# Optimization experiments

Measured on AMD Instinct MI355X. Metric: run time of the kernel, lower is better.

## Reference

```python
import jax, jax.numpy as jnp
import numpy as np

NUM_HEADS = 8

def setup_inputs() -> dict:
    key = jax.random.key(0)
    k1, k2, k3 = jax.random.split(key, 3)
    B, N, C = 4, 4096, 512
    x = jax.random.normal(k1, (B, N, C), dtype=jnp.float32)
    w_qkv = jax.random.normal(k2, (C, 3 * C), dtype=jnp.float32) * (1.0 / np.sqrt(C))
    w_proj = jax.random.normal(k3, (C, C), dtype=jnp.float32) * (1.0 / np.sqrt(C))
    b_proj = jnp.zeros((C,), dtype=jnp.float32)
    return {"x": x, "w_qkv": w_qkv, "w_proj": w_proj, "b_proj": b_proj}

def reference(x, w_qkv, w_proj, b_proj):
    B, N, C = x.shape
    H = NUM_HEADS
    D = C // H
    # qkv projection (no bias), split into q, k, v of shape [B, H, N, D]
    qkv = (x @ w_qkv).reshape(B, N, 3, H, D)
    qkv = jnp.transpose(qkv, (2, 0, 3, 1, 4))
    q, k, v = qkv[0], qkv[1], qkv[2]
    # q: softmax over head_dim; k: elu(k)+1 then softmax over sequence dim
    q = jax.nn.softmax(q, axis=-1)
    k = jax.nn.softmax(jax.nn.elu(k) + 1.0, axis=-2)
    # linear attention: context = k^T @ v  -> [B, H, D, D]
    context = jnp.einsum('bhnd,bhne->bhde', k, v)
    # out = q @ context -> [B, H, N, D]
    out = jnp.einsum('bhnd,bhde->bhne', q, context)
    out = jnp.transpose(out, (0, 2, 1, 3)).reshape(B, N, C)
    # output projection (dropout with p=0.0 is identity)
    return out @ w_proj + b_proj
```

## Files before the change

kernel.cpp:

```cpp
#include <hip/hip_runtime.h>
#include <hip/hip_bf16.h>

typedef unsigned short u16;
typedef __attribute__((ext_vector_type(8))) short bhalf8;
typedef __attribute__((ext_vector_type(4))) float fx4;

struct __align__(8) US4 { u16 v[4]; };

__device__ __forceinline__ u16 f2bf(float x) {
  union { float f; unsigned int u; } c; c.f = x;
  unsigned int r = c.u + 0x7FFFu + ((c.u >> 16) & 1u);
  return (u16)(r >> 16);
}

__device__ __forceinline__ float bf2f(u16 v) {
  union { unsigned int u; float f; } c; c.u = ((unsigned int)v) << 16;
  return c.f;
}

__device__ __forceinline__ void gload16(const void* g, void* l) {
  __builtin_amdgcn_global_load_lds((const __attribute__((address_space(1))) void*)g,
                                   (__attribute__((address_space(3))) void*)l,
                                   16, 0, 0);
}

#define MFMA16(a, b, c) __builtin_amdgcn_mfma_f32_16x16x32_bf16((a), (b), (c), 0, 0, 0)

__global__ __launch_bounds__(256)
void k_prep(const float* __restrict__ x, u16* __restrict__ xb,
            const float* __restrict__ wqkv, u16* __restrict__ wqT,
            const float* __restrict__ wproj, u16* __restrict__ wpT) {
  __shared__ float tile[64][65];
  const int bx = blockIdx.x;
  const int t = threadIdx.x;
  if (bx < 8192) {
    int i = bx * 256 + t;
    float4 v = ((const float4*)x)[i];
    US4 o;
    o.v[0] = f2bf(v.x); o.v[1] = f2bf(v.y); o.v[2] = f2bf(v.z); o.v[3] = f2bf(v.w);
    ((US4*)xb)[i] = o;
    return;
  }
  const float* in; u16* out; int C, remap, bx2;
  if (bx < 8384) { in = wqkv; out = wqT; C = 1536; remap = 1; bx2 = bx - 8192; }
  else           { in = wproj; out = wpT; C = 512;  remap = 0; bx2 = bx - 8384; }
  const int rt = bx2 & 7, ct = bx2 >> 3;
  const int r0 = rt * 64, c0 = ct * 64;
  #pragma unroll
  for (int i = 0; i < 16; ++i) {
    int e = i * 256 + t;
    int rr = e >> 6, cc = e & 63;
    tile[rr][cc] = in[(r0 + rr) * C + c0 + cc];
  }
  __syncthreads();
  #pragma unroll
  for (int i = 0; i < 16; ++i) {
    int e = i * 256 + t;
    int rr = e >> 6, cc = e & 63;
    int orow = c0 + rr;
    if (remap && orow >= 512) {
      int region = (orow - 512) >> 9;
      int within = (orow - 512) & 511;
      int h = within >> 6;
      orow = 512 + h * 128 + region * 64 + (within & 63);
    }
    out[orow * 512 + r0 + cc] = f2bf(tile[cc][rr]);
  }
}

__device__ __forceinline__ void gemm_core(const char* Ab, const char* Bb,
                                          char* As, char* Bs, fx4 acc[4][4]) {
  const int t = threadIdx.x;
  const int w = t >> 6, l = t & 63;
  const int wm = w >> 1, wn = w & 1;
  #pragma unroll 1
  for (int kt = 0; kt < 8; ++kt) {
    __syncthreads();
    const int kb = kt * 128;
    #pragma unroll
    for (int j = 0; j < 4; ++j) {
      int off = ((j * 4 + w) * 64 + l) * 16;
      int row = off >> 7;
      int colb = off & 127;
      int scol = colb ^ ((row & 7) << 4);
      gload16(Ab + row * 1024 + kb + scol, As + off);
      gload16(Bb + row * 1024 + kb + scol, Bs + off);
    }
    asm volatile("s_waitcnt vmcnt(0)" ::: "memory");
    __syncthreads();
    #pragma unroll
    for (int ks = 0; ks < 2; ++ks) {
      bhalf8 af[4], bfv[4];
      const int kbyte = ks * 64 + ((l >> 4) * 16);
      #pragma unroll
      for (int f = 0; f < 4; ++f) {
        int ra = wm * 64 + f * 16 + (l & 15);
        af[f] = *(const bhalf8*)(As + ra * 128 + (kbyte ^ ((ra & 7) << 4)));
        int rb = wn * 64 + f * 16 + (l & 15);
        bfv[f] = *(const bhalf8*)(Bs + rb * 128 + (kbyte ^ ((rb & 7) << 4)));
      }
      #pragma unroll
      for (int fm = 0; fm < 4; ++fm)
        #pragma unroll
        for (int fn = 0; fn < 4; ++fn)
          acc[fm][fn] = MFMA16(af[fm], bfv[fn], acc[fm][fn]);
    }
  }
}

__global__ __launch_bounds__(256, 2)
void k_qkv_gemm(const char* __restrict__ xb, const char* __restrict__ wqT,
                u16* __restrict__ qhat, u16* __restrict__ ctx_part,
                float* __restrict__ z_part) {
  __shared__ __align__(16) char lds[32768];
  const int bx = blockIdx.x;
  const int tM = bx & 127, tN = bx >> 7;
  fx4 acc[4][4];
  const fx4 z4 = {0.f, 0.f, 0.f, 0.f};
  #pragma unroll
  for (int i = 0; i < 4; ++i)
    #pragma unroll
    for (int j = 0; j < 4; ++j) acc[i][j] = z4;

  gemm_core(xb + tM * 131072, wqT + tN * 131072, lds, lds + 16384, acc);

  const int t = threadIdx.x, w = t >> 6, l = t & 63;
  const int wm = w >> 1, wn = w & 1;
  const int m0 = tM * 128 + wm * 64;
  const int c0 = tN * 128 + wn * 64;

  if (tN < 4) {
    #pragma unroll
    for (int fm = 0; fm < 4; ++fm) {
      #pragma unroll
      for (int fn = 0; fn < 4; ++fn)
        #pragma unroll
        for (int r = 0; r < 4; ++r)
          acc[fm][fn][r] = __expf(acc[fm][fn][r]);
      fx4 s = acc[fm][0] + acc[fm][1] + acc[fm][2] + acc[fm][3];
      fx4 inv;
      #pragma unroll
      for (int r = 0; r < 4; ++r) {
        float sv = s[r];
        sv += __shfl_xor(sv, 1, 64);
        sv += __shfl_xor(sv, 2, 64);
        sv += __shfl_xor(sv, 4, 64);
        sv += __shfl_xor(sv, 8, 64);
        inv[r] = 1.0f / sv;
      }
      #pragma unroll
      for (int fn = 0; fn < 4; ++fn)
        #pragma unroll
        for (int r = 0; r < 4; ++r) {
          int m = m0 + fm * 16 + ((l >> 4) * 4) + r;
          int c = c0 + fn * 16 + (l & 15);
          qhat[m * 512 + c] = f2bf(acc[fm][fn][r] * inv[r]);
        }
    }
  } else {
    const int h = tN - 4;
    const int b = tM >> 5;
    const int mt = tM & 31;
    const int bh = b * 8 + h;
    char* ktb = lds;
    char* vtb = lds + 16384;
    __syncthreads();
    {
      char* dstb = (wn == 0) ? ktb : vtb;
      const bool isK = (wn == 0);
      #pragma unroll
      for (int fm = 0; fm < 4; ++fm)
        #pragma unroll
        for (int fn = 0; fn < 4; ++fn) {
          int d = fn * 16 + (l & 15);
          int n0 = wm * 64 + fm * 16 + ((l >> 4) * 4);
          US4 p;
          #pragma unroll
          for (int r = 0; r < 4; ++r) {
            float v = acc[fm][fn][r];
            if (isK) { float tt = v > 0.f ? v + 1.f : __expf(v); v = __expf(tt); }
            p.v[r] = f2bf(v);
          }
          *(US4*)(dstb + d * 256 + ((2 * n0) ^ ((d & 7) << 4))) = p;
        }
    }
    __syncthreads();
    fx4 cacc[4]; fx4 zacc = z4;
    #pragma unroll
    for (int fn = 0; fn < 4; ++fn) cacc[fn] = z4;
    bhalf8 ones;
    #pragma unroll
    for (int i = 0; i < 8; ++i) ones[i] = (short)0x3F80;
    #pragma unroll
    for (int kk = 0; kk < 4; ++kk) {
      int nbyte = kk * 64 + ((l >> 4) * 16);
      int d = w * 16 + (l & 15);
      bhalf8 a = *(const bhalf8*)(ktb + d * 256 + (nbyte ^ ((d & 7) << 4)));
      #pragma unroll
      for (int fn = 0; fn < 4; ++fn) {
        int e = fn * 16 + (l & 15);
        bhalf8 bv = *(const bhalf8*)(vtb + e * 256 + (nbyte ^ ((e & 7) << 4)));
        cacc[fn] = MFMA16(a, bv, cacc[fn]);
      }
      zacc = MFMA16(a, ones, zacc);
    }
    u16* cp = ctx_part + (bh * 32 + mt) * 4096;
    #pragma unroll
    for (int fn = 0; fn < 4; ++fn)
      #pragma unroll
      for (int r = 0; r < 4; ++r) {
        int d = w * 16 + ((l >> 4) * 4) + r;
        int e = fn * 16 + (l & 15);
        cp[d * 64 + e] = f2bf(cacc[fn][r]);
      }
    if ((l & 15) == 0) {
      #pragma unroll
      for (int r = 0; r < 4; ++r)
        z_part[(bh * 32 + mt) * 64 + w * 16 + ((l >> 4) * 4) + r] = zacc[r];
    }
  }
}

__global__ __launch_bounds__(256)
void k_reduce(const u16* __restrict__ ctx_part, float* __restrict__ ctx32) {
  const int bid = blockIdx.x;
  const int bh = bid >> 2;
  const int idx0 = (bid & 3) * 1024 + threadIdx.x * 4;
  float s0 = 0.f, s1 = 0.f, s2 = 0.f, s3 = 0.f;
  #pragma unroll
  for (int mt = 0; mt < 32; ++mt) {
    US4 p = *(const US4*)(ctx_part + (bh * 32 + mt) * 4096 + idx0);
    s0 += bf2f(p.v[0]); s1 += bf2f(p.v[1]); s2 += bf2f(p.v[2]); s3 += bf2f(p.v[3]);
  }
  float4 o; o.x = s0; o.y = s1; o.z = s2; o.w = s3;
  *(float4*)(ctx32 + bh * 4096 + idx0) = o;
}

__global__ __launch_bounds__(256, 1)
void k_w2(const float* __restrict__ ctx32, const float* __restrict__ z_part,
          const u16* __restrict__ wpT, u16* __restrict__ W2T) {
  const int bh = blockIdx.x;
  const int b = bh >> 3, h = bh & 7;
  __shared__ float zinv[64];
  __shared__ __align__(16) u16 alds[64][72];
  const int t = threadIdx.x;
  if (t < 64) {
    float zs = 0.f;
    #pragma unroll
    for (int mt = 0; mt < 32; ++mt) zs += z_part[(bh * 32 + mt) * 64 + t];
    zinv[t] = 1.0f / zs;
  }
  __syncthreads();
  #pragma unroll
  for (int i = 0; i < 16; ++i) {
    int idx = i * 256 + t;
    int d = idx >> 6, e = idx & 63;
    alds[d][e] = f2bf(ctx32[bh * 4096 + idx] * zinv[d]);
  }
  __syncthreads();
  const int w = t >> 6, l = t & 63;
  fx4 acc[4][8];
  const fx4 z4 = {0.f, 0.f, 0.f, 0.f};
  #pragma unroll
  for (int i = 0; i < 4; ++i)
    #pragma unroll
    for (int j = 0; j < 8; ++j) acc[i][j] = z4;
  #pragma unroll
  for (int ks = 0; ks < 2; ++ks) {
    bhalf8 af[4];
    #pragma unroll
    for (int fm = 0; fm < 4; ++fm) {
      int row = fm * 16 + (l & 15);
      af[fm] = *(const bhalf8*)((const char*)alds + row * 144 + ks * 64 + ((l >> 4) * 16));
    }
    #pragma unroll
    for (int fn = 0; fn < 8; ++fn) {
      int c = w * 128 + fn * 16 + (l & 15);
      bhalf8 bv = *(const bhalf8*)(wpT + c * 512 + h * 64 + ks * 32 + ((l >> 4) * 8));
      #pragma unroll
      for (int fm = 0; fm < 4; ++fm)
        acc[fm][fn] = MFMA16(af[fm], bv, acc[fm][fn]);
    }
  }
  #pragma unroll
  for (int fm = 0; fm < 4; ++fm)
    #pragma unroll
    for (int fn = 0; fn < 8; ++fn) {
      int c = w * 128 + fn * 16 + (l & 15);
      int d0 = fm * 16 + ((l >> 4) * 4);
      US4 p;
      #pragma unroll
      for (int r = 0; r < 4; ++r) p.v[r] = f2bf(acc[fm][fn][r]);
      *(US4*)(W2T + (b * 512 + c) * 512 + h * 64 + d0) = p;
    }
}

__global__ __launch_bounds__(256, 2)
void k_out_gemm(const char* __restrict__ qhat, const char* __restrict__ W2T,
                const float* __restrict__ bproj, float* __restrict__ outp) {
  __shared__ __align__(16) char lds[32768];
  const int bx = blockIdx.x;
  const int tM = bx & 127, tN = bx >> 7;
  const int b = tM >> 5;
  fx4 acc[4][4];
  const fx4 z4 = {0.f, 0.f, 0.f, 0.f};
  #pragma unroll
  for (int i = 0; i < 4; ++i)
    #pragma unroll
    for (int j = 0; j < 4; ++j) acc[i][j] = z4;

  gemm_core(qhat + tM * 131072, W2T + b * 524288 + tN * 131072, lds, lds + 16384, acc);

  const int t = threadIdx.x, w = t >> 6, l = t & 63;
  const int wm = w >> 1, wn = w & 1;
  const int m0 = tM * 128 + wm * 64;
  const int c0 = tN * 128 + wn * 64;
  #pragma unroll
  for (int fm = 0; fm < 4; ++fm)
    #pragma unroll
    for (int fn = 0; fn < 4; ++fn) {
      int c = c0 + fn * 16 + (l & 15);
      float bp = bproj[c];
      #pragma unroll
      for (int r = 0; r < 4; ++r) {
        int m = m0 + fm * 16 + ((l >> 4) * 4) + r;
        outp[m * 512 + c] = acc[fm][fn][r] + bp;
      }
    }
}

extern "C" void kernel_launch(void* const* d_in, const int* in_sizes, int n_in,
                              void* d_out, int out_size, void* d_ws, size_t ws_size,
                              hipStream_t stream) {
  (void)in_sizes; (void)n_in; (void)out_size;
  const float* x     = (const float*)d_in[0];
  const float* wqkv  = (const float*)d_in[1];
  const float* wproj = (const float*)d_in[2];
  const float* bproj = (const float*)d_in[3];
  float* outp = (float*)d_out;
  char* ws = (char*)d_ws;

  char* xb   = ws;
  char* wqT  = ws + 16777216;
  char* wpT  = ws + 18350080;
  char* qhat = ws + 18874368;
  char* ctxp = ws + 35651584;
  char* zp   = ws + 44040192;
  char* ctx32= ws + 44302336;
  char* w2t  = ws + 44826624;
  if (ws_size < 46923776) return;

  k_prep<<<8448, 256, 0, stream>>>(x, (u16*)xb, wqkv, (u16*)wqT, wproj, (u16*)wpT);
  k_qkv_gemm<<<1536, 256, 0, stream>>>(xb, wqT, (u16*)qhat, (u16*)ctxp, (float*)zp);
  k_reduce<<<128, 256, 0, stream>>>((const u16*)ctxp, (float*)ctx32);
  k_w2<<<32, 256, 0, stream>>>((const float*)ctx32, (const float*)zp, (const u16*)wpT, (u16*)w2t);
  k_out_gemm<<<512, 256, 0, stream>>>(qhat, w2t, bproj, outp);
}
```

Before: 79.48 us.

## Widen GEMM tiles to 128x256 in QKV and output projection kernels

Doubles the N dimension of each GEMM block tile from 128 to 256, so every wave computes a 64x128 sub-tile with 4x8 MFMA accumulators. This halves the grid sizes and improves A-operand reuse. The QKV epilogue is restructured so each block handles a head pair, splitting K/V staging across LDS halves and computing per-head context partials with two waves per head. The cost is double the accumulator registers and more LDS (64KB/48KB), which may lower occupancy under launch_bounds(256,2). Fewer blocks may also underfill the CUs.

```diff
diff --git a/kernel.cpp b/kernel.cpp
--- a/kernel.cpp
+++ b/kernel.cpp
@@ -69,7 +69,7 @@
 }
 
 __device__ __forceinline__ void gemm_core(const char* Ab, const char* Bb,
-                                          char* As, char* Bs, fx4 acc[4][4]) {
+                                          char* As, char* Bs, fx4 acc[4][8]) {
   const int t = threadIdx.x;
   const int w = t >> 6, l = t & 63;
   const int wm = w >> 1, wn = w & 1;
@@ -78,31 +78,39 @@
     __syncthreads();
     const int kb = kt * 128;
     #pragma unroll
-    for (int j = 0; j < 4; ++j) {
-      int off = ((j * 4 + w) * 64 + l) * 16;
+    for (int i = 0; i < 4; ++i) {
+      int off = (i * 256 + t) * 16;
       int row = off >> 7;
-      int colb = off & 127;
-      int scol = colb ^ ((row & 7) << 4);
+      int scol = (off & 127) ^ ((row & 7) << 4);
       gload16(Ab + row * 1024 + kb + scol, As + off);
+    }
+    #pragma unroll
+    for (int i = 0; i < 8; ++i) {
+      int off = (i * 256 + t) * 16;
+      int row = off >> 7;
+      int scol = (off & 127) ^ ((row & 7) << 4);
       gload16(Bb + row * 1024 + kb + scol, Bs + off);
     }
     asm volatile("s_waitcnt vmcnt(0)" ::: "memory");
     __syncthreads();
     #pragma unroll
     for (int ks = 0; ks < 2; ++ks) {
-      bhalf8 af[4], bfv[4];
+      bhalf8 af[4], bfv[8];
       const int kbyte = ks * 64 + ((l >> 4) * 16);
       #pragma unroll
       for (int f = 0; f < 4; ++f) {
         int ra = wm * 64 + f * 16 + (l & 15);
         af[f] = *(const bhalf8*)(As + ra * 128 + (kbyte ^ ((ra & 7) << 4)));
-        int rb = wn * 64 + f * 16 + (l & 15);
+      }
+      #pragma unroll
+      for (int f = 0; f < 8; ++f) {
+        int rb = wn * 128 + f * 16 + (l & 15);
         bfv[f] = *(const bhalf8*)(Bs + rb * 128 + (kbyte ^ ((rb & 7) << 4)));
       }
       #pragma unroll
       for (int fm = 0; fm < 4; ++fm)
         #pragma unroll
-        for (int fn = 0; fn < 4; ++fn)
+        for (int fn = 0; fn < 8; ++fn)
           acc[fm][fn] = MFMA16(af[fm], bfv[fn], acc[fm][fn]);
     }
   }
@@ -112,111 +120,124 @@
 void k_qkv_gemm(const char* __restrict__ xb, const char* __restrict__ wqT,
                 u16* __restrict__ qhat, u16* __restrict__ ctx_part,
                 float* __restrict__ z_part) {
-  __shared__ __align__(16) char lds[32768];
+  __shared__ __align__(16) char lds[65536];
   const int bx = blockIdx.x;
   const int tM = bx & 127, tN = bx >> 7;
-  fx4 acc[4][4];
+  fx4 acc[4][8];
   const fx4 z4 = {0.f, 0.f, 0.f, 0.f};
   #pragma unroll
   for (int i = 0; i < 4; ++i)
     #pragma unroll
-    for (int j = 0; j < 4; ++j) acc[i][j] = z4;
-
-  gemm_core(xb + tM * 131072, wqT + tN * 131072, lds, lds + 16384, acc);
+    for (int j = 0; j < 8; ++j) acc[i][j] = z4;
+
+  gemm_core(xb + tM * 131072, wqT + tN * 262144, lds, lds + 16384, acc);
 
   const int t = threadIdx.x, w = t >> 6, l = t & 63;
   const int wm = w >> 1, wn = w & 1;
   const int m0 = tM * 128 + wm * 64;
-  const int c0 = tN * 128 + wn * 64;
-
-  if (tN < 4) {
+  const int c0 = tN * 256 + wn * 128;
+
+  if (tN < 2) {
     #pragma unroll
     for (int fm = 0; fm < 4; ++fm) {
       #pragma unroll
-      for (int fn = 0; fn < 4; ++fn)
+      for (int fn = 0; fn < 8; ++fn)
         #pragma unroll
         for (int r = 0; r < 4; ++r)
           acc[fm][fn][r] = __expf(acc[fm][fn][r]);
-      fx4 s = acc[fm][0] + acc[fm][1] + acc[fm][2] + acc[fm][3];
-      fx4 inv;
+      fx4 sA = acc[fm][0] + acc[fm][1] + acc[fm][2] + acc[fm][3];
+      fx4 sB = acc[fm][4] + acc[fm][5] + acc[fm][6] + acc[fm][7];
+      fx4 iA, iB;
       #pragma unroll
       for (int r = 0; r < 4; ++r) {
-        float sv = s[r];
-        sv += __shfl_xor(sv, 1, 64);
-        sv += __shfl_xor(sv, 2, 64);
-        sv += __shfl_xor(sv, 4, 64);
-        sv += __shfl_xor(sv, 8, 64);
-        inv[r] = 1.0f / sv;
-      }
-      #pragma unroll
-      for (int fn = 0; fn < 4; ++fn)
+        float a = sA[r], b = sB[r];
+        a += __shfl_xor(a, 1, 64); b += __shfl_xor(b, 1, 64);
+        a += __shfl_xor(a, 2, 64); b += __shfl_xor(b, 2, 64);
+        a += __shfl_xor(a, 4, 64); b += __shfl_xor(b, 4, 64);
+        a += __shfl_xor(a, 8, 64); b += __shfl_xor(b, 8, 64);
+        iA[r] = 1.0f / a; iB[r] = 1.0f / b;
+      }
+      #pragma unroll
+      for (int fn = 0; fn < 8; ++fn)
         #pragma unroll
         for (int r = 0; r < 4; ++r) {
           int m = m0 + fm * 16 + ((l >> 4) * 4) + r;
           int c = c0 + fn * 16 + (l & 15);
-          qhat[m * 512 + c] = f2bf(acc[fm][fn][r] * inv[r]);
+          float inv = (fn < 4) ? iA[r] : iB[r];
+          qhat[m * 512 + c] = f2bf(acc[fm][fn][r] * inv);
         }
     }
   } else {
-    const int h = tN - 4;
+    const int hpair = tN - 2;
     const int b = tM >> 5;
     const int mt = tM & 31;
-    const int bh = b * 8 + h;
-    char* ktb = lds;
-    char* vtb = lds + 16384;
+    char* ktb = lds + wn * 32768;
+    char* vtb = ktb + 16384;
     __syncthreads();
-    {
-      char* dstb = (wn == 0) ? ktb : vtb;
-      const bool isK = (wn == 0);
-      #pragma unroll
-      for (int fm = 0; fm < 4; ++fm)
-        #pragma unroll
-        for (int fn = 0; fn < 4; ++fn) {
-          int d = fn * 16 + (l & 15);
-          int n0 = wm * 64 + fm * 16 + ((l >> 4) * 4);
-          US4 p;
-          #pragma unroll
-          for (int r = 0; r < 4; ++r) {
-            float v = acc[fm][fn][r];
-            if (isK) { float tt = v > 0.f ? v + 1.f : __expf(v); v = __expf(tt); }
-            p.v[r] = f2bf(v);
-          }
-          *(US4*)(dstb + d * 256 + ((2 * n0) ^ ((d & 7) << 4))) = p;
+    #pragma unroll
+    for (int fm = 0; fm < 4; ++fm)
+      #pragma unroll
+      for (int fn = 0; fn < 8; ++fn) {
+        const bool isK = (fn < 4);
+        int d = (fn & 3) * 16 + (l & 15);
+        int n0 = wm * 64 + fm * 16 + ((l >> 4) * 4);
+        US4 p;
+        #pragma unroll
+        for (int r = 0; r < 4; ++r) {
+          float v = acc[fm][fn][r];
+          if (isK) { float tt = v > 0.f ? v + 1.f : __expf(v); v = __expf(tt); }
+          p.v[r] = f2bf(v);
         }
-    }
+        *(US4*)((isK ? ktb : vtb) + d * 256 + ((2 * n0) ^ ((d & 7) << 4))) = p;
+      }
     __syncthreads();
-    fx4 cacc[4]; fx4 zacc = z4;
-    #pragma unroll
-    for (int fn = 0; fn < 4; ++fn) cacc[fn] = z4;
+    const int hl = w >> 1;
+    const int bh = b * 8 + hpair * 2 + hl;
+    char* kb2 = lds + hl * 32768;
+    char* vb2 = kb2 + 16384;
+    fx4 cacc[2][4]; fx4 zacc[2];
+    #pragma unroll
+    for (int fd = 0; fd < 2; ++fd) {
+      zacc[fd] = z4;
+      #pragma unroll
+      for (int fe = 0; fe < 4; ++fe) cacc[fd][fe] = z4;
+    }
     bhalf8 ones;
     #pragma unroll
     for (int i = 0; i < 8; ++i) ones[i] = (short)0x3F80;
     #pragma unroll
     for (int kk = 0; kk < 4; ++kk) {
       int nbyte = kk * 64 + ((l >> 4) * 16);
-      int d = w * 16 + (l & 15);
-      bhalf8 a = *(const bhalf8*)(ktb + d * 256 + (nbyte ^ ((d & 7) << 4)));
-      #pragma unroll
-      for (int fn = 0; fn < 4; ++fn) {
-        int e = fn * 16 + (l & 15);
-        bhalf8 bv = *(const bhalf8*)(vtb + e * 256 + (nbyte ^ ((e & 7) << 4)));
-        cacc[fn] = MFMA16(a, bv, cacc[fn]);
-      }
-      zacc = MFMA16(a, ones, zacc);
+      #pragma unroll
+      for (int fd = 0; fd < 2; ++fd) {
+        int d = (w & 1) * 32 + fd * 16 + (l & 15);
+        bhalf8 a = *(const bhalf8*)(kb2 + d * 256 + (nbyte ^ ((d & 7) << 4)));
+        #pragma unroll
+        for (int fe = 0; fe < 4; ++fe) {
+          int e = fe * 16 + (l & 15);
+          bhalf8 bv = *(const bhalf8*)(vb2 + e * 256 + (nbyte ^ ((e & 7) << 4)));
+          cacc[fd][fe] = MFMA16(a, bv, cacc[fd][fe]);
+        }
+        zacc[fd] = MFMA16(a, ones, zacc[fd]);
+      }
     }
     u16* cp = ctx_part + (bh * 32 + mt) * 4096;
     #pragma unroll
-    for (int fn = 0; fn < 4; ++fn)
-      #pragma unroll
-      for (int r = 0; r < 4; ++r) {
-        int d = w * 16 + ((l >> 4) * 4) + r;
-        int e = fn * 16 + (l & 15);
-        cp[d * 64 + e] = f2bf(cacc[fn][r]);
-      }
+    for (int fd = 0; fd < 2; ++fd)
+      #pragma unroll
+      for (int fe = 0; fe < 4; ++fe)
+        #pragma unroll
+        for (int r = 0; r < 4; ++r) {
+          int d = (w & 1) * 32 + fd * 16 + ((l >> 4) * 4) + r;
+          int e = fe * 16 + (l & 15);
+          cp[d * 64 + e] = f2bf(cacc[fd][fe][r]);
+        }
     if ((l & 15) == 0) {
       #pragma unroll
-      for (int r = 0; r < 4; ++r)
-        z_part[(bh * 32 + mt) * 64 + w * 16 + ((l >> 4) * 4) + r] = zacc[r];
+      for (int fd = 0; fd < 2; ++fd)
+        #pragma unroll
+        for (int r = 0; r < 4; ++r)
+          z_part[(bh * 32 + mt) * 64 + (w & 1) * 32 + fd * 16 + ((l >> 4) * 4) + r] = zacc[fd][r];
     }
   }
 }
@@ -298,27 +319,27 @@
 __global__ __launch_bounds__(256, 2)
 void k_out_gemm(const char* __restrict__ qhat, const char* __restrict__ W2T,
                 const float* __restrict__ bproj, float* __restrict__ outp) {
-  __shared__ __align__(16) char lds[32768];
+  __shared__ __align__(16) char lds[49152];
   const int bx = blockIdx.x;
   const int tM = bx & 127, tN = bx >> 7;
   const int b = tM >> 5;
-  fx4 acc[4][4];
+  fx4 acc[4][8];
   const fx4 z4 = {0.f, 0.f, 0.f, 0.f};
   #pragma unroll
   for (int i = 0; i < 4; ++i)
     #pragma unroll
-    for (int j = 0; j < 4; ++j) acc[i][j] = z4;
-
-  gemm_core(qhat + tM * 131072, W2T + b * 524288 + tN * 131072, lds, lds + 16384, acc);
+    for (int j = 0; j < 8; ++j) acc[i][j] = z4;
+
+  gemm_core(qhat + tM * 131072, W2T + b * 524288 + tN * 262144, lds, lds + 16384, acc);
 
   const int t = threadIdx.x, w = t >> 6, l = t & 63;
   const int wm = w >> 1, wn = w & 1;
   const int m0 = tM * 128 + wm * 64;
-  const int c0 = tN * 128 + wn * 64;
+  const int c0 = tN * 256 + wn * 128;
   #pragma unroll
   for (int fm = 0; fm < 4; ++fm)
     #pragma unroll
-    for (int fn = 0; fn < 4; ++fn) {
+    for (int fn = 0; fn < 8; ++fn) {
       int c = c0 + fn * 16 + (l & 15);
       float bp = bproj[c];
       #pragma unroll
@@ -351,8 +372,8 @@
   if (ws_size < 46923776) return;
 
   k_prep<<<8448, 256, 0, stream>>>(x, (u16*)xb, wqkv, (u16*)wqT, wproj, (u16*)wpT);
-  k_qkv_gemm<<<1536, 256, 0, stream>>>(xb, wqT, (u16*)qhat, (u16*)ctxp, (float*)zp);
+  k_qkv_gemm<<<768, 256, 0, stream>>>(xb, wqT, (u16*)qhat, (u16*)ctxp, (float*)zp);
   k_reduce<<<128, 256, 0, stream>>>((const u16*)ctxp, (float*)ctx32);
   k_w2<<<32, 256, 0, stream>>>((const float*)ctx32, (const float*)zp, (const u16*)wpT, (u16*)w2t);
-  k_out_gemm<<<512, 256, 0, stream>>>(qhat, w2t, bproj, outp);
-}
+  k_out_gemm<<<256, 256, 0, stream>>>(qhat, w2t, bproj, outp);
+}
```

After: 83.40 us. 1.05x slower.

## Widen QKV GEMM tiles to 128x256 with 512-thread blocks

Applied to the files above, without the earlier changes.

The QKV projection GEMM now uses 512-thread blocks computing 128x256 output tiles, so each loaded A tile (x rows) is reused across twice as many output columns and the grid is halved. The K/V epilogue is restructured so each block handles two heads, with separate LDS regions per head for the k^T v context and the normalizer partials. LDS use per block doubles to 64KB, and the launch bound asks for 4 blocks per CU, which may limit occupancy or register budget. The output GEMM keeps the old 256-thread core.

```diff
diff --git a/kernel.cpp b/kernel.cpp
--- a/kernel.cpp
+++ b/kernel.cpp
@@ -68,8 +68,53 @@
   }
 }
 
-__device__ __forceinline__ void gemm_core(const char* Ab, const char* Bb,
-                                          char* As, char* Bs, fx4 acc[4][4]) {
+__device__ __forceinline__ void gemm_core512(const char* Ab, const char* Bb,
+                                             char* As, char* Bs, fx4 acc[4][4]) {
+  const int t = threadIdx.x;
+  const int w = t >> 6, l = t & 63;
+  const int wm = w >> 2, wn = w & 3;
+  #pragma unroll 1
+  for (int kt = 0; kt < 8; ++kt) {
+    __syncthreads();
+    const int kb = kt * 128;
+    #pragma unroll
+    for (int i = 0; i < 2; ++i) {
+      int off = (i * 512 + t) * 16;
+      int row = off >> 7;
+      int scol = (off & 127) ^ ((row & 7) << 4);
+      gload16(Ab + row * 1024 + kb + scol, As + off);
+    }
+    #pragma unroll
+    for (int i = 0; i < 4; ++i) {
+      int off = (i * 512 + t) * 16;
+      int row = off >> 7;
+      int scol = (off & 127) ^ ((row & 7) << 4);
+      gload16(Bb + row * 1024 + kb + scol, Bs + off);
+    }
+    asm volatile("s_waitcnt vmcnt(0)" ::: "memory");
+    __syncthreads();
+    #pragma unroll
+    for (int ks = 0; ks < 2; ++ks) {
+      bhalf8 af[4], bfv[4];
+      const int kbyte = ks * 64 + ((l >> 4) * 16);
+      #pragma unroll
+      for (int f = 0; f < 4; ++f) {
+        int ra = wm * 64 + f * 16 + (l & 15);
+        af[f] = *(const bhalf8*)(As + ra * 128 + (kbyte ^ ((ra & 7) << 4)));
+        int rb = wn * 64 + f * 16 + (l & 15);
+        bfv[f] = *(const bhalf8*)(Bs + rb * 128 + (kbyte ^ ((rb & 7) << 4)));
+      }
+      #pragma unroll
+      for (int fm = 0; fm < 4; ++fm)
+        #pragma unroll
+        for (int fn = 0; fn < 4; ++fn)
+          acc[fm][fn] = MFMA16(af[fm], bfv[fn], acc[fm][fn]);
+    }
+  }
+}
+
+__device__ __forceinline__ void gemm_core256(const char* Ab, const char* Bb,
+                                             char* As, char* Bs, fx4 acc[4][4]) {
   const int t = threadIdx.x;
   const int w = t >> 6, l = t & 63;
   const int wm = w >> 1, wn = w & 1;
@@ -81,8 +126,7 @@
     for (int j = 0; j < 4; ++j) {
       int off = ((j * 4 + w) * 64 + l) * 16;
       int row = off >> 7;
-      int colb = off & 127;
-      int scol = colb ^ ((row & 7) << 4);
+      int scol = (off & 127) ^ ((row & 7) << 4);
       gload16(Ab + row * 1024 + kb + scol, As + off);
       gload16(Bb + row * 1024 + kb + scol, Bs + off);
     }
@@ -108,11 +152,11 @@
   }
 }
 
-__global__ __launch_bounds__(256, 2)
+__global__ __launch_bounds__(512, 4)
 void k_qkv_gemm(const char* __restrict__ xb, const char* __restrict__ wqT,
                 u16* __restrict__ qhat, u16* __restrict__ ctx_part,
                 float* __restrict__ z_part) {
-  __shared__ __align__(16) char lds[32768];
+  __shared__ __align__(16) char lds[65536];
   const int bx = blockIdx.x;
   const int tM = bx & 127, tN = bx >> 7;
   fx4 acc[4][4];
@@ -122,14 +166,14 @@
     #pragma unroll
     for (int j = 0; j < 4; ++j) acc[i][j] = z4;
 
-  gemm_core(xb + tM * 131072, wqT + tN * 131072, lds, lds + 16384, acc);
+  gemm_core512(xb + tM * 131072, wqT + tN * 262144, lds, lds + 16384, acc);
 
   const int t = threadIdx.x, w = t >> 6, l = t & 63;
-  const int wm = w >> 1, wn = w & 1;
+  const int wm = w >> 2, wn = w & 3;
   const int m0 = tM * 128 + wm * 64;
-  const int c0 = tN * 128 + wn * 64;
-
-  if (tN < 4) {
+  const int c0 = tN * 256 + wn * 64;
+
+  if (tN < 2) {
     #pragma unroll
     for (int fm = 0; fm < 4; ++fm) {
       #pragma unroll
@@ -158,65 +202,68 @@
         }
     }
   } else {
-    const int h = tN - 4;
+    const int hpair = tN - 2;
     const int b = tM >> 5;
     const int mt = tM & 31;
-    const int bh = b * 8 + h;
-    char* ktb = lds;
-    char* vtb = lds + 16384;
-    __syncthreads();
-    {
-      char* dstb = (wn == 0) ? ktb : vtb;
-      const bool isK = (wn == 0);
-      #pragma unroll
-      for (int fm = 0; fm < 4; ++fm)
+    const int hl = wn >> 1;
+    const bool isK = ((wn & 1) == 0);
+    char* ktb = lds + hl * 32768;
+    char* vtb = ktb + 16384;
+    char* dstb = isK ? ktb : vtb;
+    __syncthreads();
+    #pragma unroll
+    for (int fm = 0; fm < 4; ++fm)
+      #pragma unroll
+      for (int fn = 0; fn < 4; ++fn) {
+        int d = fn * 16 + (l & 15);
+        int n0 = wm * 64 + fm * 16 + ((l >> 4) * 4);
+        US4 p;
         #pragma unroll
-        for (int fn = 0; fn < 4; ++fn) {
-          int d = fn * 16 + (l & 15);
-          int n0 = wm * 64 + fm * 16 + ((l >> 4) * 4);
-          US4 p;
-          #pragma unroll
-          for (int r = 0; r < 4; ++r) {
-            float v = acc[fm][fn][r];
-            if (isK) { float tt = v > 0.f ? v + 1.f : __expf(v); v = __expf(tt); }
-            p.v[r] = f2bf(v);
-          }
-          *(US4*)(dstb + d * 256 + ((2 * n0) ^ ((d & 7) << 4))) = p;
+        for (int r = 0; r < 4; ++r) {
+          float v = acc[fm][fn][r];
+          if (isK) { float tt = v > 0.f ? v + 1.f : __expf(v); v = __expf(tt); }
+          p.v[r] = f2bf(v);
         }
-    }
-    __syncthreads();
+        *(US4*)(dstb + d * 256 + ((2 * n0) ^ ((d & 7) << 4))) = p;
+      }
+    __syncthreads();
+    const int hl2 = w >> 2;
+    const int bh = b * 8 + hpair * 2 + hl2;
+    char* kb2 = lds + hl2 * 32768;
+    char* vb2 = kb2 + 16384;
+    const int d0 = (w & 3) * 16;
     fx4 cacc[4]; fx4 zacc = z4;
     #pragma unroll
-    for (int fn = 0; fn < 4; ++fn) cacc[fn] = z4;
+    for (int fe = 0; fe < 4; ++fe) cacc[fe] = z4;
     bhalf8 ones;
     #pragma unroll
     for (int i = 0; i < 8; ++i) ones[i] = (short)0x3F80;
     #pragma unroll
     for (int kk = 0; kk < 4; ++kk) {
       int nbyte = kk * 64 + ((l >> 4) * 16);
-      int d = w * 16 + (l & 15);
-      bhalf8 a = *(const bhalf8*)(ktb + d * 256 + (nbyte ^ ((d & 7) << 4)));
-      #pragma unroll
-      for (int fn = 0; fn < 4; ++fn) {
-        int e = fn * 16 + (l & 15);
-        bhalf8 bv = *(const bhalf8*)(vtb + e * 256 + (nbyte ^ ((e & 7) << 4)));
-        cacc[fn] = MFMA16(a, bv, cacc[fn]);
+      int d = d0 + (l & 15);
+      bhalf8 a = *(const bhalf8*)(kb2 + d * 256 + (nbyte ^ ((d & 7) << 4)));
+      #pragma unroll
+      for (int fe = 0; fe < 4; ++fe) {
+        int e = fe * 16 + (l & 15);
+        bhalf8 bv = *(const bhalf8*)(vb2 + e * 256 + (nbyte ^ ((e & 7) << 4)));
+        cacc[fe] = MFMA16(a, bv, cacc[fe]);
       }
       zacc = MFMA16(a, ones, zacc);
     }
     u16* cp = ctx_part + (bh * 32 + mt) * 4096;
     #pragma unroll
-    for (int fn = 0; fn < 4; ++fn)
+    for (int fe = 0; fe < 4; ++fe)
       #pragma unroll
       for (int r = 0; r < 4; ++r) {
-        int d = w * 16 + ((l >> 4) * 4) + r;
-        int e = fn * 16 + (l & 15);
-        cp[d * 64 + e] = f2bf(cacc[fn][r]);
+        int d = d0 + ((l >> 4) * 4) + r;
+        int e = fe * 16 + (l & 15);
+        cp[d * 64 + e] = f2bf(cacc[fe][r]);
       }
     if ((l & 15) == 0) {
       #pragma unroll
       for (int r = 0; r < 4; ++r)
-        z_part[(bh * 32 + mt) * 64 + w * 16 + ((l >> 4) * 4) + r] = zacc[r];
+        z_part[(bh * 32 + mt) * 64 + d0 + ((l >> 4) * 4) + r] = zacc[r];
     }
   }
 }
@@ -309,7 +356,7 @@
     #pragma unroll
     for (int j = 0; j < 4; ++j) acc[i][j] = z4;
 
-  gemm_core(qhat + tM * 131072, W2T + b * 524288 + tN * 131072, lds, lds + 16384, acc);
+  gemm_core256(qhat + tM * 131072, W2T + b * 524288 + tN * 131072, lds, lds + 16384, acc);
 
   const int t = threadIdx.x, w = t >> 6, l = t & 63;
   const int wm = w >> 1, wn = w & 1;
@@ -351,7 +398,7 @@
   if (ws_size < 46923776) return;
 
   k_prep<<<8448, 256, 0, stream>>>(x, (u16*)xb, wqkv, (u16*)wqT, wproj, (u16*)wpT);
-  k_qkv_gemm<<<1536, 256, 0, stream>>>(xb, wqT, (u16*)qhat, (u16*)ctxp, (float*)zp);
+  k_qkv_gemm<<<768, 512, 0, stream>>>(xb, wqT, (u16*)qhat, (u16*)ctxp, (float*)zp);
   k_reduce<<<128, 256, 0, stream>>>((const u16*)ctxp, (float*)ctx32);
   k_w2<<<32, 256, 0, stream>>>((const float*)ctx32, (const float*)zp, (const u16*)wpT, (u16*)w2t);
   k_out_gemm<<<512, 256, 0, stream>>>(qhat, w2t, bproj, outp);
```

New measurement: 80.43 us. No clear change (+1.2%).

## Double-buffer LDS tiles in QKV GEMM to overlap global loads with MFMA

Applied to the files above, without the earlier changes.

Adds a double-buffered GEMM core for the QKV projection kernel: the next K-tile is issued via global_load_lds into the alternate LDS buffer while MFMAs consume the current one, with a single wait and barrier per iteration. This is meant to hide global memory latency that the single-buffer loop exposed. LDS use per block doubles to 64KB, which may cut resident blocks per CU below the launch bound of 2 and reduce occupancy-based latency hiding.

```diff
diff --git a/kernel.cpp b/kernel.cpp
--- a/kernel.cpp
+++ b/kernel.cpp
@@ -68,6 +68,57 @@
   }
 }
 
+__device__ __forceinline__ void gemm_core_db(const char* Ab, const char* Bb,
+                                             char* lds, fx4 acc[4][4]) {
+  const int t = threadIdx.x;
+  const int w = t >> 6, l = t & 63;
+  const int wm = w >> 1, wn = w & 1;
+
+  #define STAGE_T(buf, kt) do {                                      \
+    const int kb_ = (kt) * 128;                                      \
+    char* As_ = lds + (buf) * 32768;                                 \
+    _Pragma("unroll")                                                \
+    for (int j = 0; j < 4; ++j) {                                    \
+      int off_ = ((j * 4 + w) * 64 + l) * 16;                        \
+      int row_ = off_ >> 7;                                          \
+      int scol_ = (off_ & 127) ^ ((row_ & 7) << 4);                  \
+      gload16(Ab + row_ * 1024 + kb_ + scol_, As_ + off_);           \
+      gload16(Bb + row_ * 1024 + kb_ + scol_, As_ + 16384 + off_);   \
+    }                                                                \
+  } while (0)
+
+  STAGE_T(0, 0);
+  asm volatile("s_waitcnt vmcnt(0)" ::: "memory");
+  __syncthreads();
+
+  #pragma unroll 1
+  for (int kt = 0; kt < 8; ++kt) {
+    const char* As = lds + (kt & 1) * 32768;
+    const char* Bs = As + 16384;
+    if (kt < 7) STAGE_T((kt + 1) & 1, kt + 1);
+    #pragma unroll
+    for (int ks = 0; ks < 2; ++ks) {
+      bhalf8 af[4], bfv[4];
+      const int kbyte = ks * 64 + ((l >> 4) * 16);
+      #pragma unroll
+      for (int f = 0; f < 4; ++f) {
+        int ra = wm * 64 + f * 16 + (l & 15);
+        af[f] = *(const bhalf8*)(As + ra * 128 + (kbyte ^ ((ra & 7) << 4)));
+        int rb = wn * 64 + f * 16 + (l & 15);
+        bfv[f] = *(const bhalf8*)(Bs + rb * 128 + (kbyte ^ ((rb & 7) << 4)));
+      }
+      #pragma unroll
+      for (int fm = 0; fm < 4; ++fm)
+        #pragma unroll
+        for (int fn = 0; fn < 4; ++fn)
+          acc[fm][fn] = MFMA16(af[fm], bfv[fn], acc[fm][fn]);
+    }
+    asm volatile("s_waitcnt vmcnt(0)" ::: "memory");
+    __syncthreads();
+  }
+  #undef STAGE_T
+}
+
 __device__ __forceinline__ void gemm_core(const char* Ab, const char* Bb,
                                           char* As, char* Bs, fx4 acc[4][4]) {
   const int t = threadIdx.x;
@@ -81,8 +132,7 @@
     for (int j = 0; j < 4; ++j) {
       int off = ((j * 4 + w) * 64 + l) * 16;
       int row = off >> 7;
-      int colb = off & 127;
-      int scol = colb ^ ((row & 7) << 4);
+      int scol = (off & 127) ^ ((row & 7) << 4);
       gload16(Ab + row * 1024 + kb + scol, As + off);
       gload16(Bb + row * 1024 + kb + scol, Bs + off);
     }
@@ -112,7 +162,7 @@
 void k_qkv_gemm(const char* __restrict__ xb, const char* __restrict__ wqT,
                 u16* __restrict__ qhat, u16* __restrict__ ctx_part,
                 float* __restrict__ z_part) {
-  __shared__ __align__(16) char lds[32768];
+  __shared__ __align__(16) char lds[65536];
   const int bx = blockIdx.x;
   const int tM = bx & 127, tN = bx >> 7;
   fx4 acc[4][4];
@@ -122,7 +172,7 @@
     #pragma unroll
     for (int j = 0; j < 4; ++j) acc[i][j] = z4;
 
-  gemm_core(xb + tM * 131072, wqT + tN * 131072, lds, lds + 16384, acc);
+  gemm_core_db(xb + tM * 131072, wqT + tN * 131072, lds, acc);
 
   const int t = threadIdx.x, w = t >> 6, l = t & 63;
   const int wm = w >> 1, wn = w & 1;
```

New measurement: 84.20 us. 1.06x slower.
